# Performance work log

Hardware: AMD Instinct MI355X
Metric: run time of the kernel (lower is better)

Reference implementation:

```python
import jax, jax.numpy as jnp
import numpy as np

BN_EPS = 1e-5

@jax.custom_vjp
def bsign(x):
    # forward: sign(x) (torch semantics: sign(0)=0, matched by jnp.sign)
    return jnp.sign(x)

def _bsign_fwd(x):
    return jnp.sign(x), x

def _bsign_bwd(x, g):
    # straight-through estimator: pass grad where |x| <= 1, zero elsewhere
    return (g * (jnp.abs(x) <= 1.0).astype(g.dtype),)

bsign.defvjp(_bsign_fwd, _bsign_bwd)


def setup_inputs() -> dict:
    key = jax.random.key(0)
    k1, k2 = jax.random.split(key, 2)
    B, IN, OUT = 8192, 2048, 2048
    x = jax.random.normal(k1, (B, IN), dtype=jnp.float32)
    weight = jax.random.normal(k2, (OUT, IN), dtype=jnp.float32) * 0.1
    gamma = jnp.ones((OUT,), dtype=jnp.float32)
    beta = jnp.zeros((OUT,), dtype=jnp.float32)
    return {"x": x, "weight": weight, "gamma": gamma, "beta": beta}


def reference(x, weight, gamma, beta):
    # binarize input and weight to {-1, 0, +1} via sign (STE in bwd)
    xb = bsign(x)            # [B, IN]
    wb = bsign(weight)       # [OUT, IN]
    out = xb @ wb.T          # [B, OUT] full-precision GEMM over +/-1 values
    # BatchNorm1d, training mode: normalize with biased batch statistics
    mean = jnp.mean(out, axis=0)                 # [OUT]
    var = jnp.var(out, axis=0)                   # biased (ddof=0), matches torch BN
    out = (out - mean) * jax.lax.rsqrt(var + BN_EPS) * gamma + beta
    return out
```

## Files before the change

kernel.cpp:

```cpp
#include <hip/hip_runtime.h>
#include <stdint.h>


typedef int int32x4 __attribute__((ext_vector_type(4)));

#define BM 128
#define BN 128
#define BKI 128
#define EPS_BN 1e-5f

__device__ __forceinline__ void load16_lds(const void* g, void* l) {
  __builtin_amdgcn_global_load_lds(
      (const __attribute__((address_space(1))) void*)g,
      (__attribute__((address_space(3))) void*)l,
      16, 0, 0);
}

__device__ __forceinline__ char sgn(float v) {
  return v > 0.f ? (char)1 : (v < 0.f ? (char)-1 : (char)0);
}

__global__ void binarize_kernel(const float* __restrict__ x,
                                const float* __restrict__ w,
                                char* __restrict__ Ab, char* __restrict__ Bb,
                                float* __restrict__ stats,
                                int nx4, int ntot4, int n2) {
  int idx = blockIdx.x * blockDim.x + threadIdx.x;
  if (idx < n2) stats[idx] = 0.f;
  if (idx >= ntot4) return;
  const float4* src;
  char* dst;
  int i;
  if (idx < nx4) {
    src = reinterpret_cast<const float4*>(x); dst = Ab; i = idx;
  } else {
    src = reinterpret_cast<const float4*>(w); dst = Bb; i = idx - nx4;
  }
  float4 v = src[i];
  char4 o;
  o.x = sgn(v.x); o.y = sgn(v.y); o.z = sgn(v.z); o.w = sgn(v.w);
  reinterpret_cast<char4*>(dst)[i] = o;
}

__global__ __launch_bounds__(256, 4) void gemm_i8_kernel(
    const char* __restrict__ A,
    const char* __restrict__ Bt,
    short* __restrict__ Craw,
    float* __restrict__ colSum,
    float* __restrict__ colSq,
    int M, int N, int K) {
  __shared__ __align__(16) char sA[BM * BKI];
  __shared__ __align__(16) char sB[BN * BKI];

  const int tid  = threadIdx.x;
  const int wave = tid >> 6;
  const int lane = tid & 63;

  const int nby = M / BM;
  const int rowBlock = (blockIdx.x % nby) * BM;
  const int colBlock = (blockIdx.x / nby) * BN;

  const int laneRow = lane >> 3;
  const int c       = lane & 7;
  const int swz     = ((c ^ laneRow) & 7) * 16;

  const char* Ag = A  + (size_t)(rowBlock + wave * 32 + laneRow) * K + swz;
  const char* Bg = Bt + (size_t)(colBlock + wave * 32 + laneRow) * K + swz;
  char* sAw = &sA[(wave * 32) * BKI];
  char* sBw = &sB[(wave * 32) * BKI];

  const int f    = lane & 15;
  const int quad = lane >> 4;
  const int wr = (wave >> 1) * 64;
  const int wc = (wave & 1) * 64;
  const int f7 = f & 7;

  int32x4 acc[4][4] = {};

  for (int k0 = 0; k0 < K; k0 += BKI) {
    __syncthreads();
#pragma unroll
    for (int i = 0; i < 4; ++i) {
      load16_lds(Ag + k0 + (size_t)(i * 8) * K, sAw + i * 8 * BKI);
      load16_lds(Bg + k0 + (size_t)(i * 8) * K, sBw + i * 8 * BKI);
    }
    __syncthreads();

#pragma unroll
    for (int s = 0; s < 2; ++s) {
      const int chunk = ((s * 4 + quad) ^ f7) * 16;
      int32x4 af[4], bfr[4];
#pragma unroll
      for (int mi = 0; mi < 4; ++mi)
        af[mi] = *reinterpret_cast<const int32x4*>(
            &sA[(wr + mi * 16 + f) * BKI + chunk]);
#pragma unroll
      for (int ni = 0; ni < 4; ++ni)
        bfr[ni] = *reinterpret_cast<const int32x4*>(
            &sB[(wc + ni * 16 + f) * BKI + chunk]);
#pragma unroll
      for (int mi = 0; mi < 4; ++mi)
#pragma unroll
        for (int ni = 0; ni < 4; ++ni)
          acc[mi][ni] = __builtin_amdgcn_mfma_i32_16x16x64_i8(
              af[mi], bfr[ni], acc[mi][ni], 0, 0, 0);
    }
  }

#pragma unroll
  for (int ni = 0; ni < 4; ++ni) {
    const int col = colBlock + wc + ni * 16 + f;
    float s = 0.f, sq = 0.f;
#pragma unroll
    for (int mi = 0; mi < 4; ++mi) {
      short* Cp = Craw + (size_t)(rowBlock + wr + mi * 16 + quad * 4) * N + col;
#pragma unroll
      for (int r = 0; r < 4; ++r) {
        const int v = acc[mi][ni][r];
        Cp[(size_t)r * N] = (short)v;
        const float fv = (float)v;
        s += fv;
        sq += fv * fv;
      }
    }
    s  += __shfl_xor(s, 16);  s  += __shfl_xor(s, 32);
    sq += __shfl_xor(sq, 16); sq += __shfl_xor(sq, 32);
    if (quad == 0) {
      atomicAdd(&colSum[col], s);
      atomicAdd(&colSq[col], sq);
    }
  }
}

__global__ void norm_kernel(const short* __restrict__ Craw,
                            float* __restrict__ C,
                            const float* __restrict__ colSum,
                            const float* __restrict__ colSq,
                            const float* __restrict__ gamma,
                            const float* __restrict__ beta,
                            int ncol4mask, int ncol4shift, int halfRows,
                            float invM) {
  const int idx = blockIdx.x * blockDim.x + threadIdx.x;
  const int c4  = idx & ncol4mask;
  const int row = idx >> ncol4shift;
  const int col = c4 * 4;
  const int ncol4 = ncol4mask + 1;

  const float4 sm = *reinterpret_cast<const float4*>(&colSum[col]);
  const float4 sv = *reinterpret_cast<const float4*>(&colSq[col]);
  const float4 g  = *reinterpret_cast<const float4*>(&gamma[col]);
  const float4 b  = *reinterpret_cast<const float4*>(&beta[col]);

  float4 sc, sh;
  {
    float m, vv;
    m = sm.x * invM; vv = sv.x * invM - m * m;
    sc.x = g.x * rsqrtf(vv + EPS_BN); sh.x = b.x - m * sc.x;
    m = sm.y * invM; vv = sv.y * invM - m * m;
    sc.y = g.y * rsqrtf(vv + EPS_BN); sh.y = b.y - m * sc.y;
    m = sm.z * invM; vv = sv.z * invM - m * m;
    sc.z = g.z * rsqrtf(vv + EPS_BN); sh.z = b.z - m * sc.z;
    m = sm.w * invM; vv = sv.w * invM - m * m;
    sc.w = g.w * rsqrtf(vv + EPS_BN); sh.w = b.w - m * sc.w;
  }

#pragma unroll
  for (int h = 0; h < 2; ++h) {
    const size_t e = (size_t)(row + h * halfRows) * ncol4 + c4;
    const short4 rv = reinterpret_cast<const short4*>(Craw)[e];
    float4 o;
    o.x = (float)rv.x * sc.x + sh.x;
    o.y = (float)rv.y * sc.y + sh.y;
    o.z = (float)rv.z * sc.z + sh.z;
    o.w = (float)rv.w * sc.w + sh.w;
    reinterpret_cast<float4*>(C)[e] = o;
  }
}

extern "C" void kernel_launch(void* const* d_in, const int* in_sizes, int n_in,
                              void* d_out, int out_size, void* d_ws,
                              size_t ws_size, hipStream_t stream) {
  const float* x     = (const float*)d_in[0];
  const float* w     = (const float*)d_in[1];
  const float* gamma = (const float*)d_in[2];
  const float* beta  = (const float*)d_in[3];
  float* C = (float*)d_out;

  const int N = in_sizes[2];
  const int K = in_sizes[1] / N;
  const int M = in_sizes[0] / K;

  char* ws = (char*)d_ws;
  char* Abin = ws;
  char* Bbin = ws + (size_t)M * K;
  short* Craw = (short*)(ws + (size_t)M * K + (size_t)N * K);
  float* stats = (float*)((char*)Craw + (size_t)M * N * sizeof(short));
  float* colSum = stats;
  float* colSq  = stats + N;

  {
    int nx4 = (M * K) / 4;
    int ntot4 = (M * K + N * K) / 4;
    binarize_kernel<<<(ntot4 + 255) / 256, 256, 0, stream>>>(
        x, w, Abin, Bbin, stats, nx4, ntot4, 2 * N);
  }

  const int nTiles = (M / BM) * (N / BN);
  gemm_i8_kernel<<<nTiles, 256, 0, stream>>>(Abin, Bbin, Craw, colSum, colSq,
                                             M, N, K);

  {
    int ncol4 = N / 4;
    int shift = 0;
    while ((1 << shift) < ncol4) ++shift;
    int total = (M / 2) * ncol4;
    norm_kernel<<<(total + 255) / 256, 256, 0, stream>>>(
        Craw, C, colSum, colSq, gamma, beta, ncol4 - 1, shift, M / 2,
        1.0f / (float)M);
  }
}
```

Before: 181.9 us.

## Fuse batch-norm into the int8 GEMM epilogue using a grid-wide barrier

Drops the separate normalization kernel and the int16 intermediate buffer. After the GEMM accumulates column sums and sums of squares atomically, every block waits at a global atomic barrier. It then reads the final statistics and writes normalized float output straight from its registers. This removes a full write and read of the raw GEMM result plus one kernel launch, but it depends on all 1024 blocks being resident at once (otherwise the barrier deadlocks). It also means no block can store output until every tile has finished its GEMM.

```diff
diff --git a/kernel.cpp b/kernel.cpp
--- a/kernel.cpp
+++ b/kernel.cpp
@@ -42,12 +42,15 @@
   reinterpret_cast<char4*>(dst)[i] = o;
 }
 
-__global__ __launch_bounds__(256, 4) void gemm_i8_kernel(
+__global__ __launch_bounds__(256, 4) void gemm_bn_kernel(
     const char* __restrict__ A,
     const char* __restrict__ Bt,
-    short* __restrict__ Craw,
+    float* __restrict__ C,
     float* __restrict__ colSum,
     float* __restrict__ colSq,
+    int* __restrict__ barrier,
+    const float* __restrict__ gamma,
+    const float* __restrict__ beta,
     int M, int N, int K) {
   __shared__ __align__(16) char sA[BM * BKI];
   __shared__ __align__(16) char sB[BN * BKI];
@@ -112,17 +115,13 @@
     const int col = colBlock + wc + ni * 16 + f;
     float s = 0.f, sq = 0.f;
 #pragma unroll
-    for (int mi = 0; mi < 4; ++mi) {
-      short* Cp = Craw + (size_t)(rowBlock + wr + mi * 16 + quad * 4) * N + col;
+    for (int mi = 0; mi < 4; ++mi)
 #pragma unroll
       for (int r = 0; r < 4; ++r) {
-        const int v = acc[mi][ni][r];
-        Cp[(size_t)r * N] = (short)v;
-        const float fv = (float)v;
+        const float fv = (float)acc[mi][ni][r];
         s += fv;
         sq += fv * fv;
       }
-    }
     s  += __shfl_xor(s, 16);  s  += __shfl_xor(s, 32);
     sq += __shfl_xor(sq, 16); sq += __shfl_xor(sq, 32);
     if (quad == 0) {
@@ -130,50 +129,39 @@
       atomicAdd(&colSq[col], sq);
     }
   }
-}
-
-__global__ void norm_kernel(const short* __restrict__ Craw,
-                            float* __restrict__ C,
-                            const float* __restrict__ colSum,
-                            const float* __restrict__ colSq,
-                            const float* __restrict__ gamma,
-                            const float* __restrict__ beta,
-                            int ncol4mask, int ncol4shift, int halfRows,
-                            float invM) {
-  const int idx = blockIdx.x * blockDim.x + threadIdx.x;
-  const int c4  = idx & ncol4mask;
-  const int row = idx >> ncol4shift;
-  const int col = c4 * 4;
-  const int ncol4 = ncol4mask + 1;
-
-  const float4 sm = *reinterpret_cast<const float4*>(&colSum[col]);
-  const float4 sv = *reinterpret_cast<const float4*>(&colSq[col]);
-  const float4 g  = *reinterpret_cast<const float4*>(&gamma[col]);
-  const float4 b  = *reinterpret_cast<const float4*>(&beta[col]);
-
-  float4 sc, sh;
-  {
-    float m, vv;
-    m = sm.x * invM; vv = sv.x * invM - m * m;
-    sc.x = g.x * rsqrtf(vv + EPS_BN); sh.x = b.x - m * sc.x;
-    m = sm.y * invM; vv = sv.y * invM - m * m;
-    sc.y = g.y * rsqrtf(vv + EPS_BN); sh.y = b.y - m * sc.y;
-    m = sm.z * invM; vv = sv.z * invM - m * m;
-    sc.z = g.z * rsqrtf(vv + EPS_BN); sh.z = b.z - m * sc.z;
-    m = sm.w * invM; vv = sv.w * invM - m * m;
-    sc.w = g.w * rsqrtf(vv + EPS_BN); sh.w = b.w - m * sc.w;
-  }
-
-#pragma unroll
-  for (int h = 0; h < 2; ++h) {
-    const size_t e = (size_t)(row + h * halfRows) * ncol4 + c4;
-    const short4 rv = reinterpret_cast<const short4*>(Craw)[e];
-    float4 o;
-    o.x = (float)rv.x * sc.x + sh.x;
-    o.y = (float)rv.y * sc.y + sh.y;
-    o.z = (float)rv.z * sc.z + sh.z;
-    o.w = (float)rv.w * sc.w + sh.w;
-    reinterpret_cast<float4*>(C)[e] = o;
+
+  __syncthreads();
+  if (tid == 0) {
+    __threadfence();
+    __hip_atomic_fetch_add(barrier, 1, __ATOMIC_RELEASE,
+                           __HIP_MEMORY_SCOPE_AGENT);
+    const int nblk = (int)gridDim.x;
+    while (__hip_atomic_load(barrier, __ATOMIC_ACQUIRE,
+                             __HIP_MEMORY_SCOPE_AGENT) < nblk) {
+      __builtin_amdgcn_s_sleep(2);
+    }
+  }
+  __syncthreads();
+
+  const float invM = 1.0f / (float)M;
+#pragma unroll
+  for (int ni = 0; ni < 4; ++ni) {
+    const int col = colBlock + wc + ni * 16 + f;
+    const float s  = __hip_atomic_load(&colSum[col], __ATOMIC_RELAXED,
+                                       __HIP_MEMORY_SCOPE_AGENT);
+    const float sq = __hip_atomic_load(&colSq[col], __ATOMIC_RELAXED,
+                                       __HIP_MEMORY_SCOPE_AGENT);
+    const float mu  = s * invM;
+    const float var = sq * invM - mu * mu;
+    const float sc  = gamma[col] * rsqrtf(var + EPS_BN);
+    const float sh  = beta[col] - mu * sc;
+#pragma unroll
+    for (int mi = 0; mi < 4; ++mi) {
+      float* Cp = C + (size_t)(rowBlock + wr + mi * 16 + quad * 4) * N + col;
+#pragma unroll
+      for (int r = 0; r < 4; ++r)
+        Cp[(size_t)r * N] = (float)acc[mi][ni][r] * sc + sh;
+    }
   }
 }
 
@@ -193,29 +181,21 @@
   char* ws = (char*)d_ws;
   char* Abin = ws;
   char* Bbin = ws + (size_t)M * K;
-  short* Craw = (short*)(ws + (size_t)M * K + (size_t)N * K);
-  float* stats = (float*)((char*)Craw + (size_t)M * N * sizeof(short));
+  float* stats = (float*)(ws + (size_t)M * K + (size_t)N * K);
   float* colSum = stats;
   float* colSq  = stats + N;
+  int* barrier  = (int*)(stats + 2 * N);
 
   {
     int nx4 = (M * K) / 4;
     int ntot4 = (M * K + N * K) / 4;
     binarize_kernel<<<(ntot4 + 255) / 256, 256, 0, stream>>>(
-        x, w, Abin, Bbin, stats, nx4, ntot4, 2 * N);
-  }
-
-  const int nTiles = (M / BM) * (N / BN);
-  gemm_i8_kernel<<<nTiles, 256, 0, stream>>>(Abin, Bbin, Craw, colSum, colSq,
-                                             M, N, K);
+        x, w, Abin, Bbin, stats, nx4, ntot4, 2 * N + 1);
+  }
 
   {
-    int ncol4 = N / 4;
-    int shift = 0;
-    while ((1 << shift) < ncol4) ++shift;
-    int total = (M / 2) * ncol4;
-    norm_kernel<<<(total + 255) / 256, 256, 0, stream>>>(
-        Craw, C, colSum, colSq, gamma, beta, ncol4 - 1, shift, M / 2,
-        1.0f / (float)M);
-  }
-}
+    const int nTiles = (M / BM) * (N / BN);
+    gemm_bn_kernel<<<nTiles, 256, 0, stream>>>(Abin, Bbin, C, colSum, colSq,
+                                               barrier, gamma, beta, M, N, K);
+  }
+}
```

Result: slower. 340.5 us (+87.3%).
